# Kernel optimization log

Measured on AMD Instinct MI355X. Metric: run time of the kernel, lower is better.

Reference implementation:

```python
import jax, jax.numpy as jnp
import numpy as np

NU, NI = 50000, 50000
N = NU + NI
NNZ = 1_000_000
DIM = 64          # dim_latent
FK = 4            # factor_k
DK = DIM // FK    # dim_k = 16
ITER_K = 2        # iterate_k
NUM_LAYER = 2     # len(dim_layer_list)
EPS = 1e-12


def setup_inputs() -> dict:
    key = jax.random.key(0)
    k1, k2, k3, k4 = jax.random.split(key, 4)
    # xavier-ish init scale for the embedding tables
    embed_user = jax.random.normal(k1, (NU, DIM), dtype=jnp.float32) * 0.1
    embed_item = jax.random.normal(k2, (NI, DIM), dtype=jnp.float32) * 0.1
    edge_head = jax.random.randint(k3, (NNZ,), 0, N, dtype=jnp.int32)
    edge_tail = jax.random.randint(k4, (NNZ,), 0, N, dtype=jnp.int32)
    return {"embed_user": embed_user, "embed_item": embed_item,
            "edge_head": edge_head, "edge_tail": edge_tail}


def _l2norm(x, axis=-1):
    # torch F.normalize(p=2): x / max(||x||, eps)
    return x / jnp.maximum(jnp.linalg.norm(x, axis=axis, keepdims=True), EPS)


def _dgcf_forward(embed_user, embed_item, head, tail):
    ego = jnp.concatenate([embed_user, embed_item], axis=0)  # [N, DIM]
    A_values = jnp.ones((FK, NNZ), dtype=ego.dtype)
    all_embed = [ego]

    def spmm(v, x):
        # sparse A (values v on edges head->tail) @ x : [N, DK]
        return jax.ops.segment_sum(v[:, None] * x[tail], head, num_segments=N)

    spmm_f = jax.vmap(spmm)  # over factor axis

    for _ in range(NUM_LAYER):
        # split ego into factor chunks: [FK, N, DK]
        xs = jnp.moveaxis(ego.reshape(N, FK, DK), 1, 0)
        factor_emb = None
        for t in range(ITER_K):
            # softmax over factors per edge; detached (as in torch .detach())
            vals = jax.lax.stop_gradient(jax.nn.softmax(A_values, axis=0))  # [FK, NNZ]
            # row sums of each factor adjacency -> D = diag(1/sqrt(rowsum))
            row_sum = jax.ops.segment_sum(vals.T, head, num_segments=N).T   # [FK, N]
            d = jnp.where(row_sum > 0,
                          1.0 / jnp.sqrt(jnp.maximum(row_sum, EPS)), 0.0)
            # factor_emb = D @ A @ D @ x  (three chained spmm in torch)
            y = spmm_f(vals, d[:, :, None] * xs)
            factor_emb = d[:, :, None] * y                                   # [FK, N, DK]
            # routing scores: sum over dim of normalize(h) * tanh(normalize(t))
            h = _l2norm(factor_emb[:, head, :], -1)                          # [FK, NNZ, DK]
            tt = _l2norm(xs[:, tail, :], -1)
            scores = jnp.sum(h * jnp.tanh(tt), axis=-1)                      # [FK, NNZ]
            A_values = A_values + scores
        # layer output: normalize last-iteration factor embeddings, re-concat
        layer_emb = _l2norm(factor_emb, -1)           # [FK, N, DK]
        ego = jnp.moveaxis(layer_emb, 0, 1).reshape(N, DIM)
        all_embed.append(ego)

    out = jnp.mean(jnp.stack(all_embed, axis=1), axis=1)  # [N, DIM]
    return out


def reference(embed_user, embed_item, edge_head, edge_tail):
    out = _dgcf_forward(embed_user, embed_item, edge_head, edge_tail)
    return out[:NU], out[NU:]
```

## Files before the change

kernel.cpp:

```cpp
#include <hip/hip_runtime.h>
#include <hip/hip_bf16.h>

#define NUSER 50000
#define NITEM 50000
#define NN    100000
#define NNZ_  1000000
#define DIM_  64
#define NBLK  391
#define EPB   1280

#define FL_SVC    1
#define FL_SC     2
#define FL_NEXT   8
#define FL_FIN    16
#define FL_ACONST 32
#define FL_ASTORE 64

static inline int ceil_div(int a, int b) { return (a + b - 1) / b; }

static __device__ inline float bf2f(unsigned short u) {
    return __uint_as_float(((unsigned int)u) << 16);
}
static __device__ inline unsigned short f2bf(float f) {
    unsigned int x = __float_as_uint(f);
    x += 0x7fffu + ((x >> 16) & 1u);
    return (unsigned short)(x >> 16);
}

#if __has_builtin(__builtin_amdgcn_fdot2_f32_bf16)
typedef __bf16 bf16x2_t __attribute__((ext_vector_type(2)));
static __device__ inline float dot2bf(unsigned int a, unsigned int b, float c) {
    return __builtin_amdgcn_fdot2_f32_bf16(__builtin_bit_cast(bf16x2_t, a),
                                           __builtin_bit_cast(bf16x2_t, b), c, false);
}
#else
static __device__ inline float dot2bf(unsigned int a, unsigned int b, float c) {
    return c + bf2f((unsigned short)(a & 0xffffu)) * bf2f((unsigned short)(b & 0xffffu))
             + bf2f((unsigned short)(a >> 16)) * bf2f((unsigned short)(b >> 16));
}
#endif

__global__ void k_init(const float* __restrict__ eu, const float* __restrict__ ei,
                       unsigned short* __restrict__ ego, unsigned short* __restrict__ te,
                       float* __restrict__ out) {
    int i = blockIdx.x * 256 + threadIdx.x;
    if (i >= NN * DIM_) return;
    float v = (i < NUSER * DIM_) ? eu[i] : ei[i - NUSER * DIM_];
    out[i] = v;
    ego[i] = f2bf(v);
    float s = v * v;
    s += __shfl_xor(s, 1); s += __shfl_xor(s, 2);
    s += __shfl_xor(s, 4); s += __shfl_xor(s, 8);
    float nrm = v / fmaxf(sqrtf(s), 1e-12f);
    float ex = __expf(2.0f * nrm);
    te[i] = f2bf((ex - 1.0f) / (ex + 1.0f));
}

__global__ void k_bcount(const int* __restrict__ head, int* __restrict__ bcount) {
    __shared__ int cnt[NBLK];
    int tid = threadIdx.x;
    for (int i = tid; i < NBLK; i += 256) cnt[i] = 0;
    __syncthreads();
    int e0 = blockIdx.x * EPB;
    int e1 = min(e0 + EPB, NNZ_);
    for (int e = e0 + tid; e < e1; e += 256)
        atomicAdd(&cnt[head[e] >> 8], 1);
    __syncthreads();
    for (int i = tid; i < NBLK; i += 256)
        if (cnt[i]) atomicAdd(&bcount[i], cnt[i]);
}

__global__ void k_bscan(const int* __restrict__ bcount, int* __restrict__ bucket_base,
                        int* __restrict__ bucket_cursor, int* __restrict__ row_start_end) {
    __shared__ int sh[512];
    int t = threadIdx.x;
    int v = (t < NBLK) ? bcount[t] : 0;
    sh[t] = v;
    __syncthreads();
    for (int off = 1; off < 512; off <<= 1) {
        int u = 0;
        if (t >= off) u = sh[t - off];
        __syncthreads();
        sh[t] += u;
        __syncthreads();
    }
    if (t < NBLK) {
        int base = sh[t] - v;
        bucket_base[t] = base;
        bucket_cursor[t] = base;
    }
    if (t == 511) {
        bucket_base[NBLK] = sh[511];
        row_start_end[0] = sh[511];
    }
}

__global__ void k_binscat(const int* __restrict__ head, const int* __restrict__ tail,
                          int* __restrict__ bucket_cursor, int2* __restrict__ bin) {
    __shared__ int cnt[NBLK];
    __shared__ int chunk[NBLK];
    int tid = threadIdx.x;
    for (int i = tid; i < NBLK; i += 256) cnt[i] = 0;
    __syncthreads();
    int e0 = blockIdx.x * EPB;
    int e1 = min(e0 + EPB, NNZ_);
    for (int e = e0 + tid; e < e1; e += 256)
        atomicAdd(&cnt[head[e] >> 8], 1);
    __syncthreads();
    for (int i = tid; i < NBLK; i += 256) {
        chunk[i] = cnt[i] ? atomicAdd(&bucket_cursor[i], cnt[i]) : 0;
        cnt[i] = 0;
    }
    __syncthreads();
    for (int e = e0 + tid; e < e1; e += 256) {
        int h = head[e], t = tail[e];
        int b = h >> 8;
        int off = atomicAdd(&cnt[b], 1);
        bin[chunk[b] + off] = make_int2(h, t);
    }
}

__global__ void k_bucket(const int2* __restrict__ bin, const int* __restrict__ bucket_base,
                         int* __restrict__ row_start, float4* __restrict__ d4a,
                         int* __restrict__ csr_tail) {
    __shared__ int deg[256];
    __shared__ int sh[256];
    __shared__ int cur[256];
    int tid = threadIdx.x;
    int b = blockIdx.x;
    int n0 = b << 8;
    int e0 = bucket_base[b], e1 = bucket_base[b + 1];
    deg[tid] = 0;
    __syncthreads();
    for (int e = e0 + tid; e < e1; e += 256)
        atomicAdd(&deg[bin[e].x - n0], 1);
    __syncthreads();
    int myDeg = deg[tid];
    sh[tid] = myDeg;
    __syncthreads();
    for (int off = 1; off < 256; off <<= 1) {
        int u = 0;
        if (tid >= off) u = sh[tid - off];
        __syncthreads();
        sh[tid] += u;
        __syncthreads();
    }
    int loff = sh[tid] - myDeg;
    int n = n0 + tid;
    if (n < NN) {
        row_start[n] = e0 + loff;
        float dd = (myDeg > 0) ? 2.0f / sqrtf((float)myDeg) : 0.0f;
        d4a[n] = make_float4(dd, dd, dd, dd);
    }
    cur[tid] = e0 + loff;
    __syncthreads();
    for (int e = e0 + tid; e < e1; e += 256) {
        int2 p = bin[e];
        int pos = atomicAdd(&cur[p.x - n0], 1);
        csr_tail[pos] = p.y;
    }
}

template<int FLAGS, int NJ>
static __device__ __forceinline__ void iter_body(
    int n, int lane, int q, int l, int f, int r0, int r1,
    unsigned short* __restrict__ svals, const float* __restrict__ d4c,
    const unsigned short* __restrict__ ego, const unsigned short* __restrict__ te,
    const int* __restrict__ csr_tail,
    float* __restrict__ A4, float* __restrict__ d4n,
    float* __restrict__ out,
    unsigned short* __restrict__ egon, unsigned short* __restrict__ ten)
{
    float ax = 0.f, ay = 0.f, az = 0.f, aw = 0.f;

    int ct[NJ]; float cw[NJ]; float ca[NJ]; uint2 cv[NJ]; float cd[NJ];
    int eb = r0 + q;
#pragma unroll
    for (int j = 0; j < NJ; ++j) {
        int i = eb + 4 * j;
        bool v = (i < r1);
        int ic = v ? i : 0;
        ct[j] = csr_tail[ic];
        float w;
        if (FLAGS & FL_SVC) w = 0.25f;
        else w = bf2f(svals[ic * 4 + f]);
        cw[j] = v ? w : 0.f;
        if ((FLAGS & FL_SC) && !(FLAGS & FL_ACONST))
            ca[j] = A4[ic * 4 + f];
    }
#pragma unroll
    for (int j = 0; j < NJ; ++j) {
        int t = ct[j];
        cd[j] = d4c[t * 4 + f];
        if (FLAGS & FL_SC)
            cv[j] = *(const uint2*)(te + t * 64 + 4 * l);
    }
#pragma unroll
    for (int j = 0; j < NJ; ++j) {
        ushort4 u = *(const ushort4*)(ego + ct[j] * 64 + 4 * l);
        float w = cw[j] * cd[j];
        ax += w * bf2f(u.x); ay += w * bf2f(u.y);
        az += w * bf2f(u.z); aw += w * bf2f(u.w);
    }

    if (NJ == 4) {
        for (int base = r0 + 16; base < r1; base += 16) {
            int tj[4]; float wj[4];
#pragma unroll
            for (int j = 0; j < 4; ++j) {
                int i = base + q + 4 * j;
                bool v = (i < r1);
                int ic = v ? i : 0;
                tj[j] = csr_tail[ic];
                float w;
                if (FLAGS & FL_SVC) w = 0.25f;
                else w = bf2f(svals[ic * 4 + f]);
                wj[j] = v ? w : 0.f;
            }
#pragma unroll
            for (int j = 0; j < 4; ++j) {
                int t = tj[j];
                float w = wj[j] * d4c[t * 4 + f];
                ushort4 u = *(const ushort4*)(ego + t * 64 + 4 * l);
                ax += w * bf2f(u.x); ay += w * bf2f(u.y);
                az += w * bf2f(u.z); aw += w * bf2f(u.w);
            }
        }
    }

    ax += __shfl_xor(ax, 16); ax += __shfl_xor(ax, 32);
    ay += __shfl_xor(ay, 16); ay += __shfl_xor(ay, 32);
    az += __shfl_xor(az, 16); az += __shfl_xor(az, 32);
    aw += __shfl_xor(aw, 16); aw += __shfl_xor(aw, 32);

    float s = ax * ax + ay * ay + az * az + aw * aw;
    s += __shfl_xor(s, 1); s += __shfl_xor(s, 2);
    float inv = 1.0f / fmaxf(sqrtf(s), 1e-12f);
    float fx = ax * inv, fy = ay * inv, fz = az * inv, fw = aw * inv;

    if (FLAGS & (FL_NEXT | FL_FIN)) {
        int src = lane >> 2;
        float t0r = __shfl(fx, src), t1r = __shfl(fy, src);
        float t2r = __shfl(fz, src), t3r = __shfl(fw, src);
        float y = (lane & 2) ? ((lane & 1) ? t3r : t2r) : ((lane & 1) ? t1r : t0r);
        int base = n * 64 + lane;
        if (FLAGS & FL_FIN) {
            out[base] = (out[base] + bf2f(ego[base]) + y) * (1.0f / 3.0f);
        }
        if (FLAGS & FL_NEXT) {
            egon[base] = f2bf(y);
            float e2 = __expf(2.0f * y);
            ten[base] = f2bf((e2 - 1.0f) / (e2 + 1.0f));
        }
    }

    if (FLAGS & FL_SC) {
        unsigned int p01 = ((unsigned int)f2bf(fy) << 16) | f2bf(fx);
        unsigned int p23 = ((unsigned int)f2bf(fw) << 16) | f2bf(fz);
        float accs = 0.f;
#pragma unroll
        for (int j = 0; j < NJ; ++j) {
            int i = eb + 4 * j;
            bool v = (i < r1);
            float dot = dot2bf(cv[j].y, p23, dot2bf(cv[j].x, p01, 0.0f));
            dot += __shfl_xor(dot, 1); dot += __shfl_xor(dot, 2);
            float a = (FLAGS & FL_ACONST) ? 1.0f : ca[j];
            a += dot;
            if ((FLAGS & FL_ASTORE) && v && (l & 3) == 0)
                A4[i * 4 + f] = a;
            float ex = __expf(a);
            float sum = ex;
            sum += __shfl_xor(sum, 4); sum += __shfl_xor(sum, 8);
            float sv = ex / sum;
            if (v && (l & 3) == 0)
                svals[i * 4 + f] = f2bf(sv);
            accs += v ? sv : 0.f;
        }
        if (NJ == 4) {
            for (int base = r0 + 16; base < r1; base += 16) {
                int tj[4]; float aj[4]; uint2 vj[4];
#pragma unroll
                for (int j = 0; j < 4; ++j) {
                    int i = base + q + 4 * j;
                    bool v = (i < r1);
                    int ic = v ? i : 0;
                    tj[j] = csr_tail[ic];
                    if (!(FLAGS & FL_ACONST)) aj[j] = A4[ic * 4 + f];
                }
#pragma unroll
                for (int j = 0; j < 4; ++j)
                    vj[j] = *(const uint2*)(te + tj[j] * 64 + 4 * l);
#pragma unroll
                for (int j = 0; j < 4; ++j) {
                    int i = base + q + 4 * j;
                    bool v = (i < r1);
                    float dot = dot2bf(vj[j].y, p23, dot2bf(vj[j].x, p01, 0.0f));
                    dot += __shfl_xor(dot, 1); dot += __shfl_xor(dot, 2);
                    float a = (FLAGS & FL_ACONST) ? 1.0f : aj[j];
                    a += dot;
                    if ((FLAGS & FL_ASTORE) && v && (l & 3) == 0)
                        A4[i * 4 + f] = a;
                    float ex = __expf(a);
                    float sum = ex;
                    sum += __shfl_xor(sum, 4); sum += __shfl_xor(sum, 8);
                    float sv = ex / sum;
                    if (v && (l & 3) == 0)
                        svals[i * 4 + f] = f2bf(sv);
                    accs += v ? sv : 0.f;
                }
            }
        }
        accs += __shfl_xor(accs, 16); accs += __shfl_xor(accs, 32);
        if (lane < 16 && (l & 3) == 0) {
            float d = (accs > 0.f) ? 1.0f / sqrtf(fmaxf(accs, 1e-12f)) : 0.f;
            d4n[n * 4 + f] = d;
        }
    }
}

template<int FLAGS>
__global__ void k_iter(unsigned short* __restrict__ svals,
                       const float* __restrict__ d4c,
                       const unsigned short* __restrict__ ego,
                       const unsigned short* __restrict__ te,
                       const int* __restrict__ row_start, const int* __restrict__ csr_tail,
                       float* __restrict__ A4,
                       float* __restrict__ d4n,
                       float* __restrict__ out,
                       unsigned short* __restrict__ egon, unsigned short* __restrict__ ten) {
    int n = (blockIdx.x * 256 + threadIdx.x) >> 6;
    if (n >= NN) return;
    int lane = threadIdx.x & 63;
    int q = lane >> 4;
    int l = lane & 15;
    int f = l >> 2;
    int r0 = __builtin_amdgcn_readfirstlane(row_start[n]);
    int r1 = __builtin_amdgcn_readfirstlane(row_start[n + 1]);
    int deg = r1 - r0;
    if (deg <= 8) {
        if (deg <= 4)
            iter_body<FLAGS, 1>(n, lane, q, l, f, r0, r1, svals, d4c, ego, te,
                                csr_tail, A4, d4n, out, egon, ten);
        else
            iter_body<FLAGS, 2>(n, lane, q, l, f, r0, r1, svals, d4c, ego, te,
                                csr_tail, A4, d4n, out, egon, ten);
    } else {
        if (deg <= 12)
            iter_body<FLAGS, 3>(n, lane, q, l, f, r0, r1, svals, d4c, ego, te,
                                csr_tail, A4, d4n, out, egon, ten);
        else
            iter_body<FLAGS, 4>(n, lane, q, l, f, r0, r1, svals, d4c, ego, te,
                                csr_tail, A4, d4n, out, egon, ten);
    }
}

extern "C" void kernel_launch(void* const* d_in, const int* in_sizes, int n_in,
                              void* d_out, int out_size, void* d_ws, size_t ws_size,
                              hipStream_t stream) {
    const float* eu = (const float*)d_in[0];
    const float* ei = (const float*)d_in[1];
    const int* head = (const int*)d_in[2];
    const int* tail = (const int*)d_in[3];
    float* out = (float*)d_out;

    float* A4 = (float*)d_ws;
    float* d4a = A4 + (size_t)NNZ_ * 4;
    float* d4b = d4a + (size_t)NN * 4;
    unsigned short* svals = (unsigned short*)(d4b + (size_t)NN * 4);
    unsigned short* ego_a = svals + (size_t)NNZ_ * 4;
    unsigned short* te_a  = ego_a + (size_t)NN * DIM_;
    unsigned short* ego_b = te_a + (size_t)NN * DIM_;
    unsigned short* te_b  = ego_b + (size_t)NN * DIM_;
    int* csr_tail = (int*)(te_b + (size_t)NN * DIM_);
    int* row_start = csr_tail + NNZ_;
    int* bcount = row_start + (NN + 1);
    int* bucket_base = bcount + NBLK;
    int* bucket_cursor = bucket_base + (NBLK + 1);
    int2* bin = (int2*)A4;

    const int node_blocks = ceil_div(NN * DIM_, 256);
    const int wave_blocks = ceil_div(NN * 64, 256);
    const int edge_pass_blocks = ceil_div(NNZ_, EPB);

    k_init<<<node_blocks, 256, 0, stream>>>(eu, ei, ego_a, te_a, out);

    hipMemsetAsync(bcount, 0, NBLK * sizeof(int), stream);
    k_bcount<<<edge_pass_blocks, 256, 0, stream>>>(head, bcount);
    k_bscan<<<1, 512, 0, stream>>>(bcount, bucket_base, bucket_cursor, &row_start[NN]);
    k_binscat<<<edge_pass_blocks, 256, 0, stream>>>(head, tail, bucket_cursor, bin);
    k_bucket<<<NBLK, 256, 0, stream>>>(bin, bucket_base, row_start, (float4*)d4a, csr_tail);

    k_iter<FL_SVC | FL_SC | FL_ACONST | FL_ASTORE><<<wave_blocks, 256, 0, stream>>>(
        svals, d4a, ego_a, te_a, row_start, csr_tail, A4, d4b, out, ego_b, te_b);

    k_iter<FL_SC | FL_ASTORE | FL_NEXT><<<wave_blocks, 256, 0, stream>>>(
        svals, d4b, ego_a, te_a, row_start, csr_tail, A4, d4a, out, ego_b, te_b);

    k_iter<FL_SC><<<wave_blocks, 256, 0, stream>>>(
        svals, d4a, ego_b, te_b, row_start, csr_tail, A4, d4b, out, ego_b, te_b);

    k_iter<FL_FIN><<<wave_blocks, 256, 0, stream>>>(
        svals, d4b, ego_b, te_b, row_start, csr_tail, A4, d4a, out, ego_b, te_b);
}
```

Measured before the change: 381.7 us.

## Pre-scale node embeddings by degree normalizer to drop per-edge d gathers

Each SpMM pass now reads a pre-multiplied table G = d*x, written by the previous pass or by init, instead of gathering the per-tail normalizer d4 for every edge and multiplying it in. The producing kernel computes its node's d from the softmax row sum and writes G for the next pass. Init is moved after bucketing so it can use the degree normalizer, and the edge-pass kernels get twice as many edges per block. This removes one random gather per edge at the cost of an extra bf16 node-table write per pass and an extra bf16 rounding of d*x.

```diff
diff --git a/kernel.cpp b/kernel.cpp
--- a/kernel.cpp
+++ b/kernel.cpp
@@ -7,7 +7,7 @@
 #define NNZ_  1000000
 #define DIM_  64
 #define NBLK  391
-#define EPB   1280
+#define EPB   2560
 
 #define FL_SVC    1
 #define FL_SC     2
@@ -15,6 +15,7 @@
 #define FL_FIN    16
 #define FL_ACONST 32
 #define FL_ASTORE 64
+#define FL_GN     128
 
 static inline int ceil_div(int a, int b) { return (a + b - 1) / b; }
 
@@ -39,22 +40,6 @@
              + bf2f((unsigned short)(a >> 16)) * bf2f((unsigned short)(b >> 16));
 }
 #endif
-
-__global__ void k_init(const float* __restrict__ eu, const float* __restrict__ ei,
-                       unsigned short* __restrict__ ego, unsigned short* __restrict__ te,
-                       float* __restrict__ out) {
-    int i = blockIdx.x * 256 + threadIdx.x;
-    if (i >= NN * DIM_) return;
-    float v = (i < NUSER * DIM_) ? eu[i] : ei[i - NUSER * DIM_];
-    out[i] = v;
-    ego[i] = f2bf(v);
-    float s = v * v;
-    s += __shfl_xor(s, 1); s += __shfl_xor(s, 2);
-    s += __shfl_xor(s, 4); s += __shfl_xor(s, 8);
-    float nrm = v / fmaxf(sqrtf(s), 1e-12f);
-    float ex = __expf(2.0f * nrm);
-    te[i] = f2bf((ex - 1.0f) / (ex + 1.0f));
-}
 
 __global__ void k_bcount(const int* __restrict__ head, int* __restrict__ bcount) {
     __shared__ int cnt[NBLK];
@@ -161,19 +146,40 @@
     }
 }
 
+__global__ void k_init(const float* __restrict__ eu, const float* __restrict__ ei,
+                       const float* __restrict__ d4a,
+                       unsigned short* __restrict__ ego, unsigned short* __restrict__ te,
+                       unsigned short* __restrict__ G0, float* __restrict__ out) {
+    int i = blockIdx.x * 256 + threadIdx.x;
+    if (i >= NN * DIM_) return;
+    float v = (i < NUSER * DIM_) ? eu[i] : ei[i - NUSER * DIM_];
+    out[i] = v;
+    ego[i] = f2bf(v);
+    G0[i] = f2bf(v * d4a[i >> 4]);
+    float s = v * v;
+    s += __shfl_xor(s, 1); s += __shfl_xor(s, 2);
+    s += __shfl_xor(s, 4); s += __shfl_xor(s, 8);
+    float nrm = v / fmaxf(sqrtf(s), 1e-12f);
+    float ex = __expf(2.0f * nrm);
+    te[i] = f2bf((ex - 1.0f) / (ex + 1.0f));
+}
+
 template<int FLAGS, int NJ>
 static __device__ __forceinline__ void iter_body(
     int n, int lane, int q, int l, int f, int r0, int r1,
-    unsigned short* __restrict__ svals, const float* __restrict__ d4c,
-    const unsigned short* __restrict__ ego, const unsigned short* __restrict__ te,
+    unsigned short* __restrict__ svals,
+    const unsigned short* __restrict__ G,
+    const unsigned short* __restrict__ te,
     const int* __restrict__ csr_tail,
-    float* __restrict__ A4, float* __restrict__ d4n,
+    float* __restrict__ A4,
     float* __restrict__ out,
+    const unsigned short* __restrict__ X,
+    unsigned short* __restrict__ Gn,
     unsigned short* __restrict__ egon, unsigned short* __restrict__ ten)
 {
     float ax = 0.f, ay = 0.f, az = 0.f, aw = 0.f;
 
-    int ct[NJ]; float cw[NJ]; float ca[NJ]; uint2 cv[NJ]; float cd[NJ];
+    int ct[NJ]; float cw[NJ]; float ca[NJ]; uint2 cv[NJ];
     int eb = r0 + q;
 #pragma unroll
     for (int j = 0; j < NJ; ++j) {
@@ -182,7 +188,7 @@
         int ic = v ? i : 0;
         ct[j] = csr_tail[ic];
         float w;
-        if (FLAGS & FL_SVC) w = 0.25f;
+        if (FLAGS & FL_SVC) w = 1.0f;
         else w = bf2f(svals[ic * 4 + f]);
         cw[j] = v ? w : 0.f;
         if ((FLAGS & FL_SC) && !(FLAGS & FL_ACONST))
@@ -190,17 +196,14 @@
     }
 #pragma unroll
     for (int j = 0; j < NJ; ++j) {
-        int t = ct[j];
-        cd[j] = d4c[t * 4 + f];
         if (FLAGS & FL_SC)
-            cv[j] = *(const uint2*)(te + t * 64 + 4 * l);
+            cv[j] = *(const uint2*)(te + ct[j] * 64 + 4 * l);
     }
 #pragma unroll
     for (int j = 0; j < NJ; ++j) {
-        ushort4 u = *(const ushort4*)(ego + ct[j] * 64 + 4 * l);
-        float w = cw[j] * cd[j];
-        ax += w * bf2f(u.x); ay += w * bf2f(u.y);
-        az += w * bf2f(u.z); aw += w * bf2f(u.w);
+        ushort4 u = *(const ushort4*)(G + ct[j] * 64 + 4 * l);
+        ax += cw[j] * bf2f(u.x); ay += cw[j] * bf2f(u.y);
+        az += cw[j] * bf2f(u.z); aw += cw[j] * bf2f(u.w);
     }
 
     if (NJ == 4) {
@@ -213,17 +216,15 @@
                 int ic = v ? i : 0;
                 tj[j] = csr_tail[ic];
                 float w;
-                if (FLAGS & FL_SVC) w = 0.25f;
+                if (FLAGS & FL_SVC) w = 1.0f;
                 else w = bf2f(svals[ic * 4 + f]);
                 wj[j] = v ? w : 0.f;
             }
 #pragma unroll
             for (int j = 0; j < 4; ++j) {
-                int t = tj[j];
-                float w = wj[j] * d4c[t * 4 + f];
-                ushort4 u = *(const ushort4*)(ego + t * 64 + 4 * l);
-                ax += w * bf2f(u.x); ay += w * bf2f(u.y);
-                az += w * bf2f(u.z); aw += w * bf2f(u.w);
+                ushort4 u = *(const ushort4*)(G + tj[j] * 64 + 4 * l);
+                ax += wj[j] * bf2f(u.x); ay += wj[j] * bf2f(u.y);
+                az += wj[j] * bf2f(u.z); aw += wj[j] * bf2f(u.w);
             }
         }
     }
@@ -238,14 +239,15 @@
     float inv = 1.0f / fmaxf(sqrtf(s), 1e-12f);
     float fx = ax * inv, fy = ay * inv, fz = az * inv, fw = aw * inv;
 
+    float y = 0.f;
     if (FLAGS & (FL_NEXT | FL_FIN)) {
         int src = lane >> 2;
         float t0r = __shfl(fx, src), t1r = __shfl(fy, src);
         float t2r = __shfl(fz, src), t3r = __shfl(fw, src);
-        float y = (lane & 2) ? ((lane & 1) ? t3r : t2r) : ((lane & 1) ? t1r : t0r);
+        y = (lane & 2) ? ((lane & 1) ? t3r : t2r) : ((lane & 1) ? t1r : t0r);
         int base = n * 64 + lane;
         if (FLAGS & FL_FIN) {
-            out[base] = (out[base] + bf2f(ego[base]) + y) * (1.0f / 3.0f);
+            out[base] = (out[base] + bf2f(X[base]) + y) * (1.0f / 3.0f);
         }
         if (FLAGS & FL_NEXT) {
             egon[base] = f2bf(y);
@@ -254,10 +256,10 @@
         }
     }
 
+    float accs = 0.f;
     if (FLAGS & FL_SC) {
         unsigned int p01 = ((unsigned int)f2bf(fy) << 16) | f2bf(fx);
         unsigned int p23 = ((unsigned int)f2bf(fw) << 16) | f2bf(fz);
-        float accs = 0.f;
 #pragma unroll
         for (int j = 0; j < NJ; ++j) {
             int i = eb + 4 * j;
@@ -266,14 +268,14 @@
             dot += __shfl_xor(dot, 1); dot += __shfl_xor(dot, 2);
             float a = (FLAGS & FL_ACONST) ? 1.0f : ca[j];
             a += dot;
-            if ((FLAGS & FL_ASTORE) && v && (l & 3) == 0)
-                A4[i * 4 + f] = a;
             float ex = __expf(a);
             float sum = ex;
             sum += __shfl_xor(sum, 4); sum += __shfl_xor(sum, 8);
             float sv = ex / sum;
-            if (v && (l & 3) == 0)
+            if (v && (l & 3) == 0) {
+                if (FLAGS & FL_ASTORE) A4[i * 4 + f] = a;
                 svals[i * 4 + f] = f2bf(sv);
+            }
             accs += v ? sv : 0.f;
         }
         if (NJ == 4) {
@@ -298,35 +300,39 @@
                     dot += __shfl_xor(dot, 1); dot += __shfl_xor(dot, 2);
                     float a = (FLAGS & FL_ACONST) ? 1.0f : aj[j];
                     a += dot;
-                    if ((FLAGS & FL_ASTORE) && v && (l & 3) == 0)
-                        A4[i * 4 + f] = a;
                     float ex = __expf(a);
                     float sum = ex;
                     sum += __shfl_xor(sum, 4); sum += __shfl_xor(sum, 8);
                     float sv = ex / sum;
-                    if (v && (l & 3) == 0)
+                    if (v && (l & 3) == 0) {
+                        if (FLAGS & FL_ASTORE) A4[i * 4 + f] = a;
                         svals[i * 4 + f] = f2bf(sv);
+                    }
                     accs += v ? sv : 0.f;
                 }
             }
         }
         accs += __shfl_xor(accs, 16); accs += __shfl_xor(accs, 32);
-        if (lane < 16 && (l & 3) == 0) {
-            float d = (accs > 0.f) ? 1.0f / sqrtf(fmaxf(accs, 1e-12f)) : 0.f;
-            d4n[n * 4 + f] = d;
-        }
+    }
+
+    if (FLAGS & (FL_GN | FL_NEXT)) {
+        float av = __shfl(accs, (lane >> 4) << 2);
+        float d = (av > 0.f) ? 1.0f / sqrtf(fmaxf(av, 1e-12f)) : 0.f;
+        int base = n * 64 + lane;
+        float src = (FLAGS & FL_NEXT) ? y : bf2f(X[base]);
+        Gn[base] = f2bf(src * d);
     }
 }
 
 template<int FLAGS>
 __global__ void k_iter(unsigned short* __restrict__ svals,
-                       const float* __restrict__ d4c,
-                       const unsigned short* __restrict__ ego,
+                       const unsigned short* __restrict__ G,
                        const unsigned short* __restrict__ te,
                        const int* __restrict__ row_start, const int* __restrict__ csr_tail,
                        float* __restrict__ A4,
-                       float* __restrict__ d4n,
                        float* __restrict__ out,
+                       const unsigned short* __restrict__ X,
+                       unsigned short* __restrict__ Gn,
                        unsigned short* __restrict__ egon, unsigned short* __restrict__ ten) {
     int n = (blockIdx.x * 256 + threadIdx.x) >> 6;
     if (n >= NN) return;
@@ -339,18 +345,18 @@
     int deg = r1 - r0;
     if (deg <= 8) {
         if (deg <= 4)
-            iter_body<FLAGS, 1>(n, lane, q, l, f, r0, r1, svals, d4c, ego, te,
-                                csr_tail, A4, d4n, out, egon, ten);
+            iter_body<FLAGS, 1>(n, lane, q, l, f, r0, r1, svals, G, te,
+                                csr_tail, A4, out, X, Gn, egon, ten);
         else
-            iter_body<FLAGS, 2>(n, lane, q, l, f, r0, r1, svals, d4c, ego, te,
-                                csr_tail, A4, d4n, out, egon, ten);
+            iter_body<FLAGS, 2>(n, lane, q, l, f, r0, r1, svals, G, te,
+                                csr_tail, A4, out, X, Gn, egon, ten);
     } else {
         if (deg <= 12)
-            iter_body<FLAGS, 3>(n, lane, q, l, f, r0, r1, svals, d4c, ego, te,
-                                csr_tail, A4, d4n, out, egon, ten);
+            iter_body<FLAGS, 3>(n, lane, q, l, f, r0, r1, svals, G, te,
+                                csr_tail, A4, out, X, Gn, egon, ten);
         else
-            iter_body<FLAGS, 4>(n, lane, q, l, f, r0, r1, svals, d4c, ego, te,
-                                csr_tail, A4, d4n, out, egon, ten);
+            iter_body<FLAGS, 4>(n, lane, q, l, f, r0, r1, svals, G, te,
+                                csr_tail, A4, out, X, Gn, egon, ten);
     }
 }
 
@@ -365,13 +371,14 @@
 
     float* A4 = (float*)d_ws;
     float* d4a = A4 + (size_t)NNZ_ * 4;
-    float* d4b = d4a + (size_t)NN * 4;
-    unsigned short* svals = (unsigned short*)(d4b + (size_t)NN * 4);
+    unsigned short* svals = (unsigned short*)(d4a + (size_t)NN * 4);
     unsigned short* ego_a = svals + (size_t)NNZ_ * 4;
     unsigned short* te_a  = ego_a + (size_t)NN * DIM_;
     unsigned short* ego_b = te_a + (size_t)NN * DIM_;
     unsigned short* te_b  = ego_b + (size_t)NN * DIM_;
-    int* csr_tail = (int*)(te_b + (size_t)NN * DIM_);
+    unsigned short* Ga    = te_b + (size_t)NN * DIM_;
+    unsigned short* Gb    = Ga + (size_t)NN * DIM_;
+    int* csr_tail = (int*)(Gb + (size_t)NN * DIM_);
     int* row_start = csr_tail + NNZ_;
     int* bcount = row_start + (NN + 1);
     int* bucket_base = bcount + NBLK;
@@ -380,25 +387,24 @@
 
     const int node_blocks = ceil_div(NN * DIM_, 256);
     const int wave_blocks = ceil_div(NN * 64, 256);
-    const int edge_pass_blocks = ceil_div(NNZ_, EPB);
-
-    k_init<<<node_blocks, 256, 0, stream>>>(eu, ei, ego_a, te_a, out);
 
     hipMemsetAsync(bcount, 0, NBLK * sizeof(int), stream);
-    k_bcount<<<edge_pass_blocks, 256, 0, stream>>>(head, bcount);
+    k_bcount<<<NBLK, 256, 0, stream>>>(head, bcount);
     k_bscan<<<1, 512, 0, stream>>>(bcount, bucket_base, bucket_cursor, &row_start[NN]);
-    k_binscat<<<edge_pass_blocks, 256, 0, stream>>>(head, tail, bucket_cursor, bin);
+    k_binscat<<<NBLK, 256, 0, stream>>>(head, tail, bucket_cursor, bin);
     k_bucket<<<NBLK, 256, 0, stream>>>(bin, bucket_base, row_start, (float4*)d4a, csr_tail);
 
-    k_iter<FL_SVC | FL_SC | FL_ACONST | FL_ASTORE><<<wave_blocks, 256, 0, stream>>>(
-        svals, d4a, ego_a, te_a, row_start, csr_tail, A4, d4b, out, ego_b, te_b);
+    k_init<<<node_blocks, 256, 0, stream>>>(eu, ei, d4a, ego_a, te_a, Ga, out);
+
+    k_iter<FL_SVC | FL_SC | FL_ACONST | FL_ASTORE | FL_GN><<<wave_blocks, 256, 0, stream>>>(
+        svals, Ga, te_a, row_start, csr_tail, A4, out, ego_a, Gb, ego_b, te_b);
 
     k_iter<FL_SC | FL_ASTORE | FL_NEXT><<<wave_blocks, 256, 0, stream>>>(
-        svals, d4b, ego_a, te_a, row_start, csr_tail, A4, d4a, out, ego_b, te_b);
-
-    k_iter<FL_SC><<<wave_blocks, 256, 0, stream>>>(
-        svals, d4a, ego_b, te_b, row_start, csr_tail, A4, d4b, out, ego_b, te_b);
+        svals, Gb, te_a, row_start, csr_tail, A4, out, ego_a, Ga, ego_b, te_b);
+
+    k_iter<FL_SC | FL_GN><<<wave_blocks, 256, 0, stream>>>(
+        svals, Ga, te_b, row_start, csr_tail, A4, out, ego_b, Gb, ego_b, te_b);
 
     k_iter<FL_FIN><<<wave_blocks, 256, 0, stream>>>(
-        svals, d4b, ego_b, te_b, row_start, csr_tail, A4, d4a, out, ego_b, te_b);
-}
+        svals, Gb, te_b, row_start, csr_tail, A4, out, ego_b, Ga, ego_b, te_b);
+}
```

Result: faster. 350.6 us (-8.1%).
